# Optimization experiments

Hardware: AMD Instinct MI355X
Metric: run time of the kernel (lower is better)

Reference implementation:

```python
import jax, jax.numpy as jnp
import numpy as np

N_NODES = 100000
IN_C = 300
OUT_C = 200
N_EDGES = 1600000
NEG_SLOPE = 0.2  # PyG GATConv default


def setup_inputs() -> dict:
    key = jax.random.key(0)
    ks = jax.random.split(key, 12)
    x = jax.random.normal(ks[0], (N_NODES, IN_C), dtype=jnp.float32)
    edge_index = jax.random.randint(ks[1], (2, N_EDGES), 0, N_NODES, dtype=jnp.int64)
    s0 = 1.0 / np.sqrt(IN_C)
    s1 = 1.0 / np.sqrt(OUT_C)
    return {
        "x": x,
        "W0": jax.random.normal(ks[2], (IN_C, OUT_C), dtype=jnp.float32) * s0,
        "a_src0": jax.random.normal(ks[3], (OUT_C,), dtype=jnp.float32) * s1,
        "a_dst0": jax.random.normal(ks[4], (OUT_C,), dtype=jnp.float32) * s1,
        "b0": jnp.zeros((OUT_C,), dtype=jnp.float32),
        "W1": jax.random.normal(ks[5], (OUT_C, OUT_C), dtype=jnp.float32) * s1,
        "a_src1": jax.random.normal(ks[6], (OUT_C,), dtype=jnp.float32) * s1,
        "a_dst1": jax.random.normal(ks[7], (OUT_C,), dtype=jnp.float32) * s1,
        "b1": jnp.zeros((OUT_C,), dtype=jnp.float32),
        "edge_index": edge_index,
    }


def _gat_conv(x, W, a_src, a_dst, b, src, dst, n):
    # h: [N, F'] projected features
    h = x @ W
    alpha_src = h @ a_src  # [N]
    alpha_dst = h @ a_dst  # [N]
    # per-edge raw attention score, message flows src -> dst
    e = jax.nn.leaky_relu(alpha_src[src] + alpha_dst[dst], NEG_SLOPE)  # [E]
    # segment softmax over incoming edges of each destination node
    m = jax.ops.segment_max(e, dst, num_segments=n)
    ex = jnp.exp(e - m[dst])
    denom = jax.ops.segment_sum(ex, dst, num_segments=n)
    alpha = ex / denom[dst]  # [E]
    # scatter-add weighted messages
    out = jax.ops.segment_sum(h[src] * alpha[:, None], dst, num_segments=n)
    return out + b


def reference(x, W0, a_src0, a_dst0, b0, W1, a_src1, a_dst1, b1, edge_index):
    n = x.shape[0]
    # PyG GATConv default: add self-loops
    loops = jnp.arange(n, dtype=edge_index.dtype)
    src = jnp.concatenate([edge_index[0], loops])
    dst = jnp.concatenate([edge_index[1], loops])
    h = jax.nn.relu(_gat_conv(x, W0, a_src0, a_dst0, b0, src, dst, n))
    h = jax.nn.relu(_gat_conv(h, W1, a_src1, a_dst1, b1, src, dst, n))
    return h
```

## Files before the change

### kernel.cpp

```cpp
#include <hip/hip_runtime.h>

#define IN_C 300
#define OUT_C 200
#define NEG_SLOPE 0.2f
#define BM 40
#define BK 20

static inline int cdiv(long a, int b) { return (int)((a + b - 1) / b); }

__global__ __launch_bounds__(256)
void zero_int_kernel(int* __restrict__ p, int n) {
  int i = blockIdx.x * blockDim.x + threadIdx.x;
  if (i < n) p[i] = 0;
}

__device__ __forceinline__ void edge_sd(const int* __restrict__ src,
                                        const int* __restrict__ dst,
                                        int i, int E, int& s, int& d) {
  if (i < E) { s = src[i]; d = dst[i]; } else { s = d = i - E; }
}

__global__ __launch_bounds__(256)
void hist_kernel(const int* __restrict__ src, const int* __restrict__ dst,
                 int E, int ET, int* __restrict__ counts) {
  int i = blockIdx.x * blockDim.x + threadIdx.x;
  if (i >= ET) return;
  int s, d; edge_sd(src, dst, i, E, s, d);
  atomicAdd(counts + d, 1);
}

__global__ __launch_bounds__(256)
void scan_a_kernel(const int* __restrict__ in, int n, int* __restrict__ out,
                   int* __restrict__ bsums) {
  __shared__ int lds[256];
  int t = threadIdx.x;
  int base = blockIdx.x * 1024 + t * 4;
  int v0 = (base + 0 < n) ? in[base + 0] : 0;
  int v1 = (base + 1 < n) ? in[base + 1] : 0;
  int v2 = (base + 2 < n) ? in[base + 2] : 0;
  int v3 = (base + 3 < n) ? in[base + 3] : 0;
  int s1 = v0 + v1, s2 = s1 + v2, s3 = s2 + v3;
  lds[t] = s3;
  __syncthreads();
  for (int o = 1; o < 256; o <<= 1) {
    int x = (t >= o) ? lds[t - o] : 0;
    __syncthreads();
    lds[t] += x;
    __syncthreads();
  }
  int pre = (t > 0) ? lds[t - 1] : 0;
  if (base + 0 < n) out[base + 0] = pre + v0;
  if (base + 1 < n) out[base + 1] = pre + s1;
  if (base + 2 < n) out[base + 2] = pre + s2;
  if (base + 3 < n) out[base + 3] = pre + s3;
  if (t == 255) bsums[blockIdx.x] = lds[255];
}

__global__ __launch_bounds__(256)
void scan_b_kernel(int* __restrict__ bs, int nb) {
  __shared__ int lds[256];
  int t = threadIdx.x;
  lds[t] = (t < nb) ? bs[t] : 0;
  __syncthreads();
  for (int o = 1; o < 256; o <<= 1) {
    int x = (t >= o) ? lds[t - o] : 0;
    __syncthreads();
    lds[t] += x;
    __syncthreads();
  }
  if (t < nb) bs[t] = lds[t];
}

__global__ __launch_bounds__(256)
void scan_c_kernel(int* __restrict__ out, int n, const int* __restrict__ bs) {
  int i = blockIdx.x * blockDim.x + threadIdx.x;
  if (i >= n) return;
  int b = i >> 10;
  if (b > 0) out[i] += bs[b - 1];
}

__global__ __launch_bounds__(256)
void fill_kernel(const int* __restrict__ src, const int* __restrict__ dst,
                 int E, int ET, const int* __restrict__ rowptr,
                 int* __restrict__ cursor, int* __restrict__ csr_src) {
  int i = blockIdx.x * blockDim.x + threadIdx.x;
  if (i >= ET) return;
  int s, d; edge_sd(src, dst, i, E, s, d);
  int pos = rowptr[d] + atomicAdd(cursor + d, 1);
  csr_src[pos] = s;
}

__global__ __launch_bounds__(256)
void gemm_tiled_kernel(const float* __restrict__ A, const float* __restrict__ W,
                       float* __restrict__ C, int K) {
  __shared__ float As[BM][BK];
  __shared__ float Ws[BK][OUT_C];
  int t = threadIdx.x;
  int rg = t / 50;
  int cg = t % 50;
  long row0 = (long)blockIdx.x * BM;

  float4 acc[8];
  #pragma unroll
  for (int i = 0; i < 8; ++i) acc[i] = make_float4(0.f, 0.f, 0.f, 0.f);

  for (int kc = 0; kc < K; kc += BK) {
    if (t < BM * (BK / 4)) {
      int r = t / (BK / 4), c = t % (BK / 4);
      *(float4*)&As[r][c * 4] = *(const float4*)(A + (row0 + r) * K + kc + c * 4);
    }
    for (int idx = t; idx < BK * (OUT_C / 4); idx += 256) {
      int r = idx / (OUT_C / 4), c = idx % (OUT_C / 4);
      *(float4*)&Ws[r][c * 4] = *(const float4*)(W + (long)(kc + r) * OUT_C + c * 4);
    }
    __syncthreads();
    if (rg < 5) {
      #pragma unroll
      for (int kk = 0; kk < BK; kk += 4) {
        float4 w0 = *(float4*)&Ws[kk + 0][cg * 4];
        float4 w1 = *(float4*)&Ws[kk + 1][cg * 4];
        float4 w2 = *(float4*)&Ws[kk + 2][cg * 4];
        float4 w3 = *(float4*)&Ws[kk + 3][cg * 4];
        #pragma unroll
        for (int i = 0; i < 8; ++i) {
          float4 a = *(float4*)&As[rg * 8 + i][kk];
          acc[i].x += a.x * w0.x + a.y * w1.x + a.z * w2.x + a.w * w3.x;
          acc[i].y += a.x * w0.y + a.y * w1.y + a.z * w2.y + a.w * w3.y;
          acc[i].z += a.x * w0.z + a.y * w1.z + a.z * w2.z + a.w * w3.z;
          acc[i].w += a.x * w0.w + a.y * w1.w + a.z * w2.w + a.w * w3.w;
        }
      }
    }
    __syncthreads();
  }
  if (rg < 5) {
    #pragma unroll
    for (int i = 0; i < 8; ++i)
      *(float4*)(C + (row0 + rg * 8 + i) * OUT_C + cg * 4) = acc[i];
  }
}

__global__ __launch_bounds__(256)
void alphas_kernel(const float* __restrict__ h, const float* __restrict__ a_src,
                   const float* __restrict__ a_dst, float* __restrict__ as_out,
                   float* __restrict__ ad_out, int N) {
  int wid = (int)(((long)blockIdx.x * blockDim.x + threadIdx.x) >> 6);
  int lane = threadIdx.x & 63;
  if (wid >= N) return;
  const float* row = h + (long)wid * OUT_C;
  float ss = 0.f, sd = 0.f;
  for (int c = lane; c < OUT_C; c += 64) {
    float v = row[c];
    ss += v * a_src[c];
    sd += v * a_dst[c];
  }
  for (int off = 32; off > 0; off >>= 1) {
    ss += __shfl_down(ss, off);
    sd += __shfl_down(sd, off);
  }
  if (lane == 0) { as_out[wid] = ss; ad_out[wid] = sd; }
}

__global__ __launch_bounds__(256)
void gather_agg_kernel(const float* __restrict__ h, const float* __restrict__ asN,
                       const float* __restrict__ adN, const int* __restrict__ rowptr,
                       const int* __restrict__ csr_src, const float* __restrict__ bias,
                       float* __restrict__ out, int N) {
  int wid = (int)(((long)blockIdx.x * blockDim.x + threadIdx.x) >> 6);
  int lane = threadIdx.x & 63;
  if (wid >= N) return;
  int start = rowptr[wid], end = rowptr[wid + 1];
  float ad = adN[wid];

  float m = -1e30f;
  for (int j = start + lane; j < end; j += 64) {
    float sc = asN[csr_src[j]] + ad;
    sc = sc > 0.f ? sc : NEG_SLOPE * sc;
    m = fmaxf(m, sc);
  }
  for (int o = 32; o > 0; o >>= 1) m = fmaxf(m, __shfl_xor(m, o));
  float se = 0.f;
  for (int j = start + lane; j < end; j += 64) {
    float sc = asN[csr_src[j]] + ad;
    sc = sc > 0.f ? sc : NEG_SLOPE * sc;
    se += __expf(sc - m);
  }
  for (int o = 32; o > 0; o >>= 1) se += __shfl_xor(se, o);
  float inv = 1.0f / se;

  float acc0 = 0.f, acc1 = 0.f, acc2 = 0.f, acc3 = 0.f;
  int c0 = lane, c1 = lane + 64, c2 = lane + 128, c3 = lane + 192;
  for (int j = start; j < end; ++j) {
    int s = csr_src[j];
    float sc = asN[s] + ad;
    sc = sc > 0.f ? sc : NEG_SLOPE * sc;
    float w = __expf(sc - m) * inv;
    const float* hrow = h + (long)s * OUT_C;
    acc0 += w * hrow[c0];
    acc1 += w * hrow[c1];
    acc2 += w * hrow[c2];
    if (c3 < OUT_C) acc3 += w * hrow[c3];
  }
  float* orow = out + (long)wid * OUT_C;
  orow[c0] = fmaxf(acc0 + bias[c0], 0.f);
  orow[c1] = fmaxf(acc1 + bias[c1], 0.f);
  orow[c2] = fmaxf(acc2 + bias[c2], 0.f);
  if (c3 < OUT_C) orow[c3] = fmaxf(acc3 + bias[c3], 0.f);
}

static void run_layer(const float* xin, int K, const float* W,
                      const float* a_s, const float* a_d, const float* b,
                      const int* rowptr, const int* csr_src, int N,
                      float* hbuf, float* asN, float* adN, float* outbuf,
                      hipStream_t stream) {
  gemm_tiled_kernel<<<N / BM, 256, 0, stream>>>(xin, W, hbuf, K);
  alphas_kernel<<<cdiv((long)N * 64, 256), 256, 0, stream>>>(hbuf, a_s, a_d, asN, adN, N);
  gather_agg_kernel<<<cdiv((long)N * 64, 256), 256, 0, stream>>>(
      hbuf, asN, adN, rowptr, csr_src, b, outbuf, N);
}

extern "C" void kernel_launch(void* const* d_in, const int* in_sizes, int n_in,
                              void* d_out, int out_size, void* d_ws, size_t ws_size,
                              hipStream_t stream) {
  const float* x   = (const float*)d_in[0];
  const float* W0  = (const float*)d_in[1];
  const float* as0 = (const float*)d_in[2];
  const float* ad0 = (const float*)d_in[3];
  const float* b0  = (const float*)d_in[4];
  const float* W1  = (const float*)d_in[5];
  const float* as1 = (const float*)d_in[6];
  const float* ad1 = (const float*)d_in[7];
  const float* b1  = (const float*)d_in[8];
  const int*   ei  = (const int*)d_in[9];

  const int N  = in_sizes[0] / IN_C;
  const int E  = in_sizes[9] / 2;
  const int ET = E + N;
  const int* src = ei;
  const int* dst = ei + E;

  float* out = (float*)d_out;

  char* ws = (char*)d_ws;
  float* hbuf   = (float*)ws;
  float* asN    = (float*)(ws + (size_t)N * OUT_C * 4);
  float* adN    = asN + N;
  int*   rowptr = (int*)(adN + N);
  int*   counts = rowptr + (N + 1);
  int*   bsums  = counts + N;
  int*   csrsrc = bsums + 256;

  const int nb = cdiv(N, 1024);

  zero_int_kernel<<<cdiv(N, 256), 256, 0, stream>>>(counts, N);
  hist_kernel<<<cdiv(ET, 256), 256, 0, stream>>>(src, dst, E, ET, counts);
  scan_a_kernel<<<nb, 256, 0, stream>>>(counts, N, rowptr + 1, bsums);
  scan_b_kernel<<<1, 256, 0, stream>>>(bsums, nb);
  scan_c_kernel<<<cdiv(N, 256), 256, 0, stream>>>(rowptr + 1, N, bsums);
  zero_int_kernel<<<1, 256, 0, stream>>>(rowptr, 1);
  zero_int_kernel<<<cdiv(N, 256), 256, 0, stream>>>(counts, N);
  fill_kernel<<<cdiv(ET, 256), 256, 0, stream>>>(src, dst, E, ET, rowptr, counts, csrsrc);

  run_layer(x, IN_C, W0, as0, ad0, b0, rowptr, csrsrc, N, hbuf, asN, adN, out, stream);
  run_layer(out, OUT_C, W1, as1, ad1, b1, rowptr, csrsrc, N, hbuf, asN, adN, out, stream);
}
```

Baseline: 1.350 ms.

## Fuse attention-score dot products into GEMM epilogue with register-prefetched tiles

The GEMM is rewritten so each wave owns 10 rows across padded 256 columns, with all 256 threads active instead of 250. The next K-chunk is prefetched into registers while the current one is being computed. The alpha_src/alpha_dst dot products are computed in the epilogue with wave shuffles, which removes the separate alphas kernel and its re-read of H. The costs are more register pressure from the prefetch buffers, a launch-bounds occupancy hint, and 56 padded columns of wasted FMA work.

```diff
diff --git a/kernel.cpp b/kernel.cpp
--- a/kernel.cpp
+++ b/kernel.cpp
@@ -3,8 +3,10 @@
 #define IN_C 300
 #define OUT_C 200
 #define NEG_SLOPE 0.2f
-#define BM 40
-#define BK 20
+
+#define BMB 40
+#define BMW 10
+#define BKC 20
 
 static inline int cdiv(long a, int b) { return (int)((a + b - 1) / b); }
 
@@ -90,75 +92,106 @@
   csr_src[pos] = s;
 }
 
-__global__ __launch_bounds__(256)
-void gemm_tiled_kernel(const float* __restrict__ A, const float* __restrict__ W,
-                       float* __restrict__ C, int K) {
-  __shared__ float As[BM][BK];
-  __shared__ float Ws[BK][OUT_C];
+__global__ __launch_bounds__(256, 4)
+void gemm_ws_kernel(const float* __restrict__ A, const float* __restrict__ W,
+                    const float* __restrict__ a_src, const float* __restrict__ a_dst,
+                    float* __restrict__ H, float* __restrict__ asN,
+                    float* __restrict__ adN, int K, int N) {
+  __shared__ float As[BMB][BKC];
+  __shared__ float Ws[BKC][256];
   int t = threadIdx.x;
-  int rg = t / 50;
-  int cg = t % 50;
-  long row0 = (long)blockIdx.x * BM;
-
-  float4 acc[8];
+  int wave = t >> 6, lane = t & 63;
+  int col = lane * 4;
+  long row0 = (long)blockIdx.x * BMB;
+  int wrow = wave * BMW;
+
+  const bool hasA = t < BMB * (BKC / 4);
+  const int ar = t / (BKC / 4), ac = t % (BKC / 4);
+
+  float4 pw[5];
+  float4 pa;
+
+  auto loadchunk = [&](int kc) {
+    #pragma unroll
+    for (int i = 0; i < 5; ++i) {
+      int idx = t + i * 256;
+      int r = idx >> 6, cs = idx & 63;
+      int c = cs * 4;
+      if (c < OUT_C)
+        pw[i] = *(const float4*)(W + (long)(kc + r) * OUT_C + c);
+      else
+        pw[i] = make_float4(0.f, 0.f, 0.f, 0.f);
+    }
+    if (hasA) {
+      long rr = row0 + ar; if (rr >= N) rr = N - 1;
+      pa = *(const float4*)(A + rr * K + kc + ac * 4);
+    }
+  };
+  auto storechunk = [&]() {
+    #pragma unroll
+    for (int i = 0; i < 5; ++i) {
+      int idx = t + i * 256;
+      int r = idx >> 6, cs = idx & 63;
+      *(float4*)&Ws[r][cs * 4] = pw[i];
+    }
+    if (hasA) *(float4*)&As[ar][ac * 4] = pa;
+  };
+
+  float4 acc[BMW];
   #pragma unroll
-  for (int i = 0; i < 8; ++i) acc[i] = make_float4(0.f, 0.f, 0.f, 0.f);
-
-  for (int kc = 0; kc < K; kc += BK) {
-    if (t < BM * (BK / 4)) {
-      int r = t / (BK / 4), c = t % (BK / 4);
-      *(float4*)&As[r][c * 4] = *(const float4*)(A + (row0 + r) * K + kc + c * 4);
-    }
-    for (int idx = t; idx < BK * (OUT_C / 4); idx += 256) {
-      int r = idx / (OUT_C / 4), c = idx % (OUT_C / 4);
-      *(float4*)&Ws[r][c * 4] = *(const float4*)(W + (long)(kc + r) * OUT_C + c * 4);
-    }
-    __syncthreads();
-    if (rg < 5) {
+  for (int r = 0; r < BMW; ++r) acc[r] = make_float4(0.f, 0.f, 0.f, 0.f);
+
+  const int nch = K / BKC;
+  loadchunk(0);
+  for (int ch = 0; ch < nch; ++ch) {
+    storechunk();
+    __syncthreads();
+    if (ch + 1 < nch) loadchunk((ch + 1) * BKC);
+    #pragma unroll
+    for (int kk = 0; kk < BKC; kk += 4) {
+      float4 w0 = *(float4*)&Ws[kk + 0][col];
+      float4 w1 = *(float4*)&Ws[kk + 1][col];
+      float4 w2 = *(float4*)&Ws[kk + 2][col];
+      float4 w3 = *(float4*)&Ws[kk + 3][col];
       #pragma unroll
-      for (int kk = 0; kk < BK; kk += 4) {
-        float4 w0 = *(float4*)&Ws[kk + 0][cg * 4];
-        float4 w1 = *(float4*)&Ws[kk + 1][cg * 4];
-        float4 w2 = *(float4*)&Ws[kk + 2][cg * 4];
-        float4 w3 = *(float4*)&Ws[kk + 3][cg * 4];
-        #pragma unroll
-        for (int i = 0; i < 8; ++i) {
-          float4 a = *(float4*)&As[rg * 8 + i][kk];
-          acc[i].x += a.x * w0.x + a.y * w1.x + a.z * w2.x + a.w * w3.x;
-          acc[i].y += a.x * w0.y + a.y * w1.y + a.z * w2.y + a.w * w3.y;
-          acc[i].z += a.x * w0.z + a.y * w1.z + a.z * w2.z + a.w * w3.z;
-          acc[i].w += a.x * w0.w + a.y * w1.w + a.z * w2.w + a.w * w3.w;
-        }
+      for (int r = 0; r < BMW; ++r) {
+        float4 a = *(float4*)&As[wrow + r][kk];
+        acc[r].x += a.x * w0.x + a.y * w1.x + a.z * w2.x + a.w * w3.x;
+        acc[r].y += a.x * w0.y + a.y * w1.y + a.z * w2.y + a.w * w3.y;
+        acc[r].z += a.x * w0.z + a.y * w1.z + a.z * w2.z + a.w * w3.z;
+        acc[r].w += a.x * w0.w + a.y * w1.w + a.z * w2.w + a.w * w3.w;
       }
     }
     __syncthreads();
   }
-  if (rg < 5) {
-    #pragma unroll
-    for (int i = 0; i < 8; ++i)
-      *(float4*)(C + (row0 + rg * 8 + i) * OUT_C + cg * 4) = acc[i];
-  }
-}
-
-__global__ __launch_bounds__(256)
-void alphas_kernel(const float* __restrict__ h, const float* __restrict__ a_src,
-                   const float* __restrict__ a_dst, float* __restrict__ as_out,
-                   float* __restrict__ ad_out, int N) {
-  int wid = (int)(((long)blockIdx.x * blockDim.x + threadIdx.x) >> 6);
-  int lane = threadIdx.x & 63;
-  if (wid >= N) return;
-  const float* row = h + (long)wid * OUT_C;
-  float ss = 0.f, sd = 0.f;
-  for (int c = lane; c < OUT_C; c += 64) {
-    float v = row[c];
-    ss += v * a_src[c];
-    sd += v * a_dst[c];
-  }
-  for (int off = 32; off > 0; off >>= 1) {
-    ss += __shfl_down(ss, off);
-    sd += __shfl_down(sd, off);
-  }
-  if (lane == 0) { as_out[wid] = ss; ad_out[wid] = sd; }
+
+  if (col < OUT_C) {
+    #pragma unroll
+    for (int r = 0; r < BMW; ++r) {
+      long grow = row0 + wrow + r;
+      if (grow < N) *(float4*)(H + grow * OUT_C + col) = acc[r];
+    }
+  }
+  float4 vs, vd;
+  if (col < OUT_C) {
+    vs = *(const float4*)(a_src + col);
+    vd = *(const float4*)(a_dst + col);
+  } else {
+    vs = make_float4(0.f, 0.f, 0.f, 0.f);
+    vd = make_float4(0.f, 0.f, 0.f, 0.f);
+  }
+  #pragma unroll
+  for (int r = 0; r < BMW; ++r) {
+    float ss = acc[r].x * vs.x + acc[r].y * vs.y + acc[r].z * vs.z + acc[r].w * vs.w;
+    float sd = acc[r].x * vd.x + acc[r].y * vd.y + acc[r].z * vd.z + acc[r].w * vd.w;
+    #pragma unroll
+    for (int o = 32; o > 0; o >>= 1) {
+      ss += __shfl_xor(ss, o);
+      sd += __shfl_xor(sd, o);
+    }
+    long grow = row0 + wrow + r;
+    if (lane == 0 && grow < N) { asN[grow] = ss; adN[grow] = sd; }
+  }
 }
 
 __global__ __launch_bounds__(256)
@@ -213,8 +246,8 @@
                       const int* rowptr, const int* csr_src, int N,
                       float* hbuf, float* asN, float* adN, float* outbuf,
                       hipStream_t stream) {
-  gemm_tiled_kernel<<<N / BM, 256, 0, stream>>>(xin, W, hbuf, K);
-  alphas_kernel<<<cdiv((long)N * 64, 256), 256, 0, stream>>>(hbuf, a_s, a_d, asN, adN, N);
+  gemm_ws_kernel<<<cdiv(N, BMB), 256, 0, stream>>>(xin, W, a_s, a_d,
+                                                   hbuf, asN, adN, K, N);
   gather_agg_kernel<<<cdiv((long)N * 64, 256), 256, 0, stream>>>(
       hbuf, asN, adN, rowptr, csr_src, b, outbuf, N);
 }
```

After: 3.640 ms. 170% more time.
